# Performance work log

Measured on AMD Instinct MI355X. Metric: run time of the kernel, lower is better.

## Reference

```python
import jax, jax.numpy as jnp
import numpy as np

B, S, D, H, I, E, K, L, C = 4, 1024, 512, 8, 2048, 8, 2, 4, 4
D2 = D // 2
EPS = 1e-5  # torch LayerNorm default


def _ln(x, w, b):
    m = jnp.mean(x, -1, keepdims=True)
    v = jnp.mean((x - m) ** 2, -1, keepdims=True)
    return (x - m) * jax.lax.rsqrt(v + EPS) * w + b


def setup_inputs() -> dict:
    key = jax.random.key(0)
    ks = iter(jax.random.split(key, 40))
    n = lambda shp, s=0.02: jax.random.normal(next(ks), shp, dtype=jnp.float32) * s
    return {
        'embeddings': jax.random.normal(next(ks), (B, S, D), jnp.float32),
        'attention_mask': jnp.ones((B, S), jnp.float32),
        'in_w': n((L, 3 * D, D)), 'in_b': jnp.zeros((L, 3 * D)),
        'out_w': n((L, D, D)), 'out_b': jnp.zeros((L, D)),
        'ln1_w': jnp.ones((L, D)), 'ln1_b': jnp.zeros((L, D)),
        'ln2_w': jnp.ones((L, D)), 'ln2_b': jnp.zeros((L, D)),
        'gate_w': n((L, E, D)),
        'e_w1': n((L, E, D, I)), 'e_b1': jnp.zeros((L, E, I)),
        'e_w2': n((L, E, I, D)), 'e_b2': jnp.zeros((L, E, D)),
        'mln_w': jnp.ones((L, D)), 'mln_b': jnp.zeros((L, D)),
        'fln_w': jnp.ones((D,)), 'fln_b': jnp.zeros((D,)),
        'pool_w': n((D, D)), 'pool_b': jnp.zeros((D,)),
        'cls_w': n((C, D)), 'cls_b': jnp.zeros((C,)),
        'cf_w1': n((D2, D)), 'cf_b1': jnp.zeros((D2,)),
        'cf_w2': n((1, D2)), 'cf_b2': jnp.zeros((1,)),
    }


def _forward(embeddings, attention_mask, in_w, in_b, out_w, out_b, ln1_w, ln1_b,
             ln2_w, ln2_b, gate_w, e_w1, e_b1, e_w2, e_b2, mln_w, mln_b,
             fln_w, fln_b, pool_w, pool_b, cls_w, cls_b, cf_w1, cf_b1, cf_w2, cf_b2):
    x = embeddings
    dh = D // H
    total_aux = jnp.float32(0.0)
    for l in range(L):
        # --- self-attention (eval mode, dropout off) ---
        h = _ln(x, ln1_w[l], ln1_b[l])
        qkv = h @ in_w[l].T + in_b[l]                       # (B,S,3D)
        q, k, v = jnp.split(qkv, 3, axis=-1)
        q = q.reshape(B, S, H, dh).transpose(0, 2, 1, 3)
        k = k.reshape(B, S, H, dh).transpose(0, 2, 1, 3)
        v = v.reshape(B, S, H, dh).transpose(0, 2, 1, 3)
        scores = jnp.einsum('bhqd,bhkd->bhqk', q, k) / (dh ** 0.5)
        attn = jax.nn.softmax(scores, axis=-1)
        ctx = jnp.einsum('bhqk,bhkd->bhqd', attn, v).transpose(0, 2, 1, 3).reshape(B, S, D)
        x = x + (ctx @ out_w[l].T + out_b[l])
        # --- MoE FFN (residual is the post-norm2 tensor, per source) ---
        h = _ln(x, ln2_w[l], ln2_b[l])
        flat = h.reshape(-1, D)                             # (T,D)
        probs = jax.nn.softmax(flat @ gate_w[l].T, axis=-1) # (T,E)
        vals, idx = jax.lax.top_k(probs, K)                 # (T,K)
        vals = vals / vals.sum(-1, keepdims=True)
        onehot = jax.nn.one_hot(idx, E, dtype=flat.dtype)   # (T,K,E)
        comb = jnp.einsum('tk,tke->te', vals, onehot)       # (T,E) per-expert weight, 0 if not selected
        mid = jax.nn.gelu(jnp.einsum('td,edf->tef', flat, e_w1[l]) + e_b1[l], approximate=False)
        eout = jnp.einsum('tef,efd->ted', mid, e_w2[l]) + e_b2[l]
        moe_out = jnp.einsum('ted,te->td', eout, comb).reshape(B, S, D)
        moe_out = moe_out * attention_mask[..., None]
        x = _ln(h + moe_out, mln_w[l], mln_b[l])
        usage = onehot.sum((0, 1)) / flat.shape[0]
        total_aux = total_aux + jnp.mean((usage - 1.0 / E) ** 2)
    # --- head ---
    x = _ln(x, fln_w, fln_b)
    me = attention_mask[..., None]
    pooled = (x * me).sum(1) / jnp.maximum(me.sum(1), 1e-9)
    pooled = jnp.tanh(pooled @ pool_w.T + pool_b)
    logits = pooled @ cls_w.T + cls_b
    conf = jax.nn.sigmoid(jax.nn.relu(pooled @ cf_w1.T + cf_b1) @ cf_w2.T + cf_b2)
    return logits, total_aux / L, conf


def reference(embeddings, attention_mask, in_w, in_b, out_w, out_b, ln1_w, ln1_b,
              ln2_w, ln2_b, gate_w, e_w1, e_b1, e_w2, e_b2, mln_w, mln_b,
              fln_w, fln_b, pool_w, pool_b, cls_w, cls_b, cf_w1, cf_b1, cf_w2, cf_b2):
    return _forward(embeddings, attention_mask, in_w, in_b, out_w, out_b, ln1_w, ln1_b,
                    ln2_w, ln2_b, gate_w, e_w1, e_b1, e_w2, e_b2, mln_w, mln_b,
                    fln_w, fln_b, pool_w, pool_b, cls_w, cls_b, cf_w1, cf_b1, cf_w2, cf_b2)
```

## Files before the change

kernel.cpp:

```cpp
#include <hip/hip_runtime.h>
#include <math.h>

#define B_ 4
#define S_ 1024
#define D_ 512
#define H_ 8
#define DH_ 64
#define I_ 2048
#define E_ 8
#define L_ 4
#define T_ 4096

using bf16x8 = __attribute__((ext_vector_type(8))) __bf16;
using f32x4  = __attribute__((ext_vector_type(4))) float;

typedef __attribute__((address_space(1))) const void gvoid;
typedef __attribute__((address_space(3))) void lvoid;
__device__ __forceinline__ void gl_lds16(const void* g, void* l){
  __builtin_amdgcn_global_load_lds((gvoid*)g, (lvoid*)l, 16, 0, 0);
}

__device__ __forceinline__ float wred_sum(float v){
#pragma unroll
  for(int m=32;m>0;m>>=1) v += __shfl_xor(v, m, 64);
  return v;
}
__device__ __forceinline__ unsigned short f2bf(float f){
  unsigned x = __float_as_uint(f);
  unsigned r = (x + 0x7FFFu + ((x>>16)&1u)) >> 16;
  return (unsigned short)r;
}
__device__ __forceinline__ float bf2f(unsigned short u){
  return __uint_as_float(((unsigned)u)<<16);
}
__device__ __forceinline__ unsigned pk2(float a, float b){
  return (unsigned)f2bf(a) | ((unsigned)f2bf(b)<<16);
}

template<int BM, int BN, bool MOE, bool GATHER, bool OUT_BF16, int ACT, bool ADD_IN>
__global__ __launch_bounds__(256)
void gemm_k(const unsigned short* __restrict__ A, const unsigned short* __restrict__ Bv,
            void* Cp, const float* __restrict__ bias, const float* addin,
            int M, int N, int K, int lda, int ldb, int ldc,
            int hdiv, long sAb, long sAh, long sBb, long sBh, long sCb, long sCh,
            float scale,
            const int* __restrict__ moff, const int* __restrict__ mcnt,
            const int* __restrict__ rowtok, const int* __restrict__ btab,
            long sBe, int biasStride)
{
  constexpr int BK = 64;
  constexpr int WM = BM/2, WN = BN/2, FM = WM/16, FNN = WN/16;
  constexpr int RPC = 2048/BK;
  constexpr int NA = BM/RPC, NB = BN/RPC;
  __shared__ unsigned short As[BM*BK];
  __shared__ unsigned short Bs[BN*BK];

  const int tid = threadIdx.x, wid = tid>>6, lane = tid&63;
  const int wy = wid>>1, wx = wid&1, ln16 = lane&15, q8 = (lane>>4)*8;
  int m0 = blockIdx.x*BM;
  const int n0 = blockIdx.y*BN;

  float* Cf = nullptr; unsigned short* Ch = nullptr;
  const float* biasp = bias;
  const unsigned short* Bp = Bv;
  int seg = 0, cnt = M;

  if constexpr (MOE){
    int tv = btab[blockIdx.x];
    if (tv < 0) return;
    int e = tv>>8;
    m0 = (tv&255)*BM;
    seg = moff[e]; cnt = mcnt[e];
    Bp = Bv + (long)e*sBe;
    if constexpr (OUT_BF16) Ch = (unsigned short*)Cp; else Cf = (float*)Cp;
    if (biasp) biasp += (long)e*biasStride;
  } else {
    int z = blockIdx.z, zb = z/hdiv, zh = z%hdiv;
    A  += (long)zb*sAb + (long)zh*sAh;
    Bp += (long)zb*sBb + (long)zh*sBh;
    long coff = (long)zb*sCb + (long)zh*sCh;
    if constexpr (OUT_BF16) Ch = (unsigned short*)Cp + coff; else Cf = ((float*)Cp) + coff;
    if constexpr (ADD_IN) addin += coff;
  }

  const int srow = tid >> 3;
  const int scol = (tid & 7) * 8;
  long ga[NA], gb[NB];
#pragma unroll
  for (int j=0; j<NA; j++){
    int r = m0 + j*RPC + srow;
    if constexpr (MOE){
      r = min(r, cnt-1);
      long gr = GATHER ? (long)rowtok[seg+r] : (long)(seg+r);
      ga[j] = gr*lda + scol;
    } else {
      ga[j] = (long)min(r, M-1)*lda + scol;
    }
  }
#pragma unroll
  for (int j=0; j<NB; j++){
    int bn = min(n0 + j*RPC + srow, N-1);
    gb[j] = (long)bn*ldb + scol;
  }

  f32x4 acc[FM][FNN];
#pragma unroll
  for(int i=0;i<FM;i++)
#pragma unroll
    for(int j=0;j<FNN;j++){ f32x4 z = {0.f,0.f,0.f,0.f}; acc[i][j] = z; }

  for (int k0 = 0; k0 < K; k0 += BK){
    __syncthreads();
#pragma unroll
    for (int j=0; j<NA; j++) gl_lds16(A + ga[j] + k0, As + j*2048 + wid*512);
#pragma unroll
    for (int j=0; j<NB; j++) gl_lds16(Bp + gb[j] + k0, Bs + j*2048 + wid*512);
    __syncthreads();
#pragma unroll
    for (int kk=0; kk<2; kk++){
      bf16x8 fa[FM], fb[FNN];
#pragma unroll
      for(int i=0;i<FM;i++) fa[i] = *(const bf16x8*)&As[(wy*WM + i*16 + ln16)*BK + kk*32 + q8];
#pragma unroll
      for(int j=0;j<FNN;j++) fb[j] = *(const bf16x8*)&Bs[(wx*WN + j*16 + ln16)*BK + kk*32 + q8];
#pragma unroll
      for(int i=0;i<FM;i++)
#pragma unroll
        for(int j=0;j<FNN;j++)
          acc[i][j] = __builtin_amdgcn_mfma_f32_16x16x32_bf16(fa[i], fb[j], acc[i][j], 0, 0, 0);
    }
  }

#pragma unroll
  for(int i=0;i<FM;i++){
    int mbase = m0 + wy*WM + i*16 + (lane>>4)*4;
#pragma unroll
    for(int j=0;j<FNN;j++){
      int n = n0 + wx*WN + j*16 + ln16;
      float bv = biasp ? biasp[n] : 0.f;
      f32x4 v = acc[i][j];
#pragma unroll
      for(int r=0;r<4;r++){
        int m = mbase + r;
        if (m < cnt){
          float x = v[r]*scale + bv;
          if constexpr (ACT == 1) x = 0.5f*x*(1.f + erff(x*0.70710678118654752f));
          long ci = (long)(MOE ? seg + m : m)*ldc + n;
          if constexpr (ADD_IN) x += addin[ci];
          if constexpr (OUT_BF16) Ch[ci] = f2bf(x);
          else Cf[ci] = x;
        }
      }
    }
  }
}

__global__ __launch_bounds__(256)
void flash_k(const unsigned short* __restrict__ qkvb, const unsigned short* __restrict__ Vt,
             unsigned short* __restrict__ ctx)
{
  __shared__ unsigned short Pl[4][16*72];
  const int qt = blockIdx.x, z = blockIdx.y, b = z>>3, h = z&7;
  const int wid = threadIdx.x>>6, lane = threadIdx.x&63;
  const int ln16 = lane&15, g = lane>>4;
  const int q0 = qt*64 + wid*16;
  unsigned short* Pw = &Pl[wid][0];

  const unsigned short* Qp = qkvb + (long)(b*1024 + q0 + ln16)*1536 + h*64 + g*8;
  bf16x8 qf0 = *(const bf16x8*)Qp;
  bf16x8 qf1 = *(const bf16x8*)(Qp + 32);
  const unsigned short* Kbase = qkvb + (long)b*1024*1536 + 512 + h*64 + g*8;
  const unsigned short* Vbase = Vt + (long)z*65536 + g*8;

  float m_s[4], l_s[4];
  f32x4 oacc[4];
#pragma unroll
  for(int r=0;r<4;r++){ m_s[r] = -1e30f; l_s[r] = 0.f; }
#pragma unroll
  for(int j=0;j<4;j++){ f32x4 zz = {0.f,0.f,0.f,0.f}; oacc[j] = zz; }

  for (int t = 0; t < 16; ++t){
    bf16x8 kf[4][2], vf[4][2];
#pragma unroll
    for(int j=0;j<4;j++){
      const unsigned short* kp = Kbase + (long)(t*64 + j*16 + ln16)*1536;
      kf[j][0] = *(const bf16x8*)kp;
      kf[j][1] = *(const bf16x8*)(kp + 32);
      const unsigned short* vp = Vbase + (long)(j*16 + ln16)*1024 + t*64;
      vf[j][0] = *(const bf16x8*)vp;
      vf[j][1] = *(const bf16x8*)(vp + 32);
    }
    f32x4 sacc[4];
#pragma unroll
    for(int j=0;j<4;j++){ f32x4 zz = {0.f,0.f,0.f,0.f}; sacc[j] = zz; }
#pragma unroll
    for(int j=0;j<4;j++){
      sacc[j] = __builtin_amdgcn_mfma_f32_16x16x32_bf16(qf0, kf[j][0], sacc[j], 0,0,0);
      sacc[j] = __builtin_amdgcn_mfma_f32_16x16x32_bf16(qf1, kf[j][1], sacc[j], 0,0,0);
    }
#pragma unroll
    for(int j=0;j<4;j++)
#pragma unroll
      for(int r=0;r<4;r++) sacc[j][r] *= 0.125f;
    float alpha[4];
#pragma unroll
    for(int r=0;r<4;r++){
      float mx = fmaxf(fmaxf(sacc[0][r], sacc[1][r]), fmaxf(sacc[2][r], sacc[3][r]));
#pragma unroll
      for(int m=1;m<16;m<<=1) mx = fmaxf(mx, __shfl_xor(mx, m, 64));
      float mn = fmaxf(m_s[r], mx);
      alpha[r] = __expf(m_s[r] - mn);
      m_s[r] = mn;
    }
#pragma unroll
    for(int j=0;j<4;j++)
#pragma unroll
      for(int r=0;r<4;r++) sacc[j][r] = __expf(sacc[j][r] - m_s[r]);
#pragma unroll
    for(int r=0;r<4;r++){
      float rs = sacc[0][r]+sacc[1][r]+sacc[2][r]+sacc[3][r];
#pragma unroll
      for(int m=1;m<16;m<<=1) rs += __shfl_xor(rs, m, 64);
      l_s[r] = l_s[r]*alpha[r] + rs;
    }
#pragma unroll
    for(int j=0;j<4;j++)
#pragma unroll
      for(int r=0;r<4;r++) oacc[j][r] *= alpha[r];
#pragma unroll
    for(int j=0;j<4;j++)
#pragma unroll
      for(int r=0;r<4;r++)
        Pw[(g*4+r)*72 + j*16 + ln16] = f2bf(sacc[j][r]);
    bf16x8 pf0 = *(const bf16x8*)&Pw[ln16*72 + g*8];
    bf16x8 pf1 = *(const bf16x8*)&Pw[ln16*72 + 32 + g*8];
#pragma unroll
    for(int j=0;j<4;j++){
      oacc[j] = __builtin_amdgcn_mfma_f32_16x16x32_bf16(pf0, vf[j][0], oacc[j], 0,0,0);
      oacc[j] = __builtin_amdgcn_mfma_f32_16x16x32_bf16(pf1, vf[j][1], oacc[j], 0,0,0);
    }
  }
#pragma unroll
  for(int r=0;r<4;r++){
    float inv = 1.f/l_s[r];
    long row = (long)(b*1024 + q0 + g*4 + r)*512 + h*64;
#pragma unroll
    for(int j=0;j<4;j++)
      ctx[row + j*16 + ln16] = f2bf(oacc[j][r]*inv);
  }
}

template<bool OUT_BF16>
__global__ __launch_bounds__(256)
void ln_w_k(const float* __restrict__ in, const float* __restrict__ w,
            const float* __restrict__ bb, void* __restrict__ outp)
{
  int row = blockIdx.x*4 + (threadIdx.x>>6), lane = threadIdx.x&63;
  const float4* p = (const float4*)(in + (long)row*512 + lane*8);
  float4 a = p[0], c = p[1];
  float s = a.x+a.y+a.z+a.w + c.x+c.y+c.z+c.w;
  float q = a.x*a.x+a.y*a.y+a.z*a.z+a.w*a.w + c.x*c.x+c.y*c.y+c.z*c.z+c.w*c.w;
  s = wred_sum(s); q = wred_sum(q);
  float mean = s*(1.f/512.f);
  float var  = q*(1.f/512.f) - mean*mean;
  float inv  = rsqrtf(var + 1e-5f);
  const float4* wp = (const float4*)(w + lane*8);
  const float4* bp = (const float4*)(bb + lane*8);
  float4 w0 = wp[0], w1 = wp[1], b0 = bp[0], b1 = bp[1];
  float o0 = (a.x-mean)*inv*w0.x + b0.x, o1 = (a.y-mean)*inv*w0.y + b0.y;
  float o2 = (a.z-mean)*inv*w0.z + b0.z, o3 = (a.w-mean)*inv*w0.w + b0.w;
  float o4 = (c.x-mean)*inv*w1.x + b1.x, o5 = (c.y-mean)*inv*w1.y + b1.y;
  float o6 = (c.z-mean)*inv*w1.z + b1.z, o7 = (c.w-mean)*inv*w1.w + b1.w;
  if constexpr (OUT_BF16){
    *(uint4*)((unsigned short*)outp + (long)row*512 + lane*8) =
      make_uint4(pk2(o0,o1), pk2(o2,o3), pk2(o4,o5), pk2(o6,o7));
  } else {
    float4* op = (float4*)((float*)outp + (long)row*512 + lane*8);
    op[0] = make_float4(o0,o1,o2,o3);
    op[1] = make_float4(o4,o5,o6,o7);
  }
}

__global__ __launch_bounds__(256)
void ln2route_k(const float* __restrict__ in, const float* __restrict__ w,
                const float* __restrict__ bb, unsigned short* __restrict__ h2,
                const float* __restrict__ gw,
                int* __restrict__ tok_e, float* __restrict__ tok_w)
{
  int tok = blockIdx.x*4 + (threadIdx.x>>6), lane = threadIdx.x&63;
  const float4* p = (const float4*)(in + (long)tok*512 + lane*8);
  float4 a = p[0], c = p[1];
  float s = a.x+a.y+a.z+a.w + c.x+c.y+c.z+c.w;
  float q = a.x*a.x+a.y*a.y+a.z*a.z+a.w*a.w + c.x*c.x+c.y*c.y+c.z*c.z+c.w*c.w;
  s = wred_sum(s); q = wred_sum(q);
  float mean = s*(1.f/512.f);
  float var  = q*(1.f/512.f) - mean*mean;
  float inv  = rsqrtf(var + 1e-5f);
  const float4* wp = (const float4*)(w + lane*8);
  const float4* bp = (const float4*)(bb + lane*8);
  float4 w0 = wp[0], w1 = wp[1], b0 = bp[0], b1 = bp[1];
  float o[8];
  o[0] = (a.x-mean)*inv*w0.x + b0.x; o[1] = (a.y-mean)*inv*w0.y + b0.y;
  o[2] = (a.z-mean)*inv*w0.z + b0.z; o[3] = (a.w-mean)*inv*w0.w + b0.w;
  o[4] = (c.x-mean)*inv*w1.x + b1.x; o[5] = (c.y-mean)*inv*w1.y + b1.y;
  o[6] = (c.z-mean)*inv*w1.z + b1.z; o[7] = (c.w-mean)*inv*w1.w + b1.w;
  *(uint4*)(h2 + (long)tok*512 + lane*8) =
    make_uint4(pk2(o[0],o[1]), pk2(o[2],o[3]), pk2(o[4],o[5]), pk2(o[6],o[7]));
  float lg[8];
#pragma unroll
  for(int e=0;e<8;e++){
    const float4* gr = (const float4*)(gw + e*512 + lane*8);
    float4 g0 = gr[0], g1 = gr[1];
    float d = o[0]*g0.x + o[1]*g0.y + o[2]*g0.z + o[3]*g0.w
            + o[4]*g1.x + o[5]*g1.y + o[6]*g1.z + o[7]*g1.w;
    lg[e] = wred_sum(d);
  }
  if (lane == 0){
    float mx = lg[0];
#pragma unroll
    for(int e=1;e<8;e++) mx = fmaxf(mx, lg[e]);
    float pr[8];
#pragma unroll
    for(int e=0;e<8;e++) pr[e] = expf(lg[e]-mx);
    int e0 = 0; float p0 = pr[0];
#pragma unroll
    for(int e=1;e<8;e++) if (pr[e] > p0){ p0 = pr[e]; e0 = e; }
    int e1 = -1; float p1 = -1.f;
#pragma unroll
    for(int e=0;e<8;e++) if (e != e0 && pr[e] > p1){ p1 = pr[e]; e1 = e; }
    float invp = 1.f/(p0+p1);
    tok_e[2*tok] = e0; tok_e[2*tok+1] = e1;
    tok_w[2*tok] = p0*invp; tok_w[2*tok+1] = p1*invp;
  }
}

__global__ __launch_bounds__(1024)
void plan_scatter_k(const int* __restrict__ tok_e, const float* __restrict__ tok_w,
                    int* __restrict__ offs, int* __restrict__ cnts, float* __restrict__ aux,
                    int* __restrict__ btab, int* __restrict__ btab64,
                    int* __restrict__ rowtok, float* __restrict__ roww, int* __restrict__ rowof)
{
  __shared__ int hist[8];
  __shared__ int offsS[8];
  __shared__ int base[8];
  const int t = threadIdx.x;
  if (t < 8) hist[t] = 0;
  __syncthreads();
  int e[8]; float w[8];
#pragma unroll
  for (int i=0;i<8;i++){
    e[i] = tok_e[t + i*1024];
    w[i] = tok_w[t + i*1024];
    atomicAdd(&hist[e[i]], 1);
  }
  __syncthreads();
  if (t == 0){
    int o = 0, idx = 0, idx2 = 0; float a = 0.f;
    for (int ee=0; ee<8; ee++){
      offsS[ee] = o;
      int c = hist[ee];
      o += c;
      float u = (float)c*(1.f/4096.f) - 0.125f;
      a += u*u;
      int nb = (c + 127) >> 7;
      for (int j=0;j<nb;j++) btab[idx++] = (ee<<8)|j;
      int nb2 = (c + 63) >> 6;
      for (int j=0;j<nb2;j++) btab64[idx2++] = (ee<<8)|j;
    }
    while (idx < 80) btab[idx++] = -1;
    while (idx2 < 144) btab64[idx2++] = -1;
    *aux += a*(1.f/8.f);
  }
  __syncthreads();
  if (t < 8){
    cnts[t] = hist[t];
    offs[t] = offsS[t];
    base[t] = offsS[t];
  }
  __syncthreads();
#pragma unroll
  for (int i=0;i<8;i++){
    int pos = atomicAdd(&base[e[i]], 1);
    int gi = t + i*1024;
    rowtok[pos] = gi>>1;
    roww[pos] = w[i];
    rowof[gi] = pos;
  }
}

__global__ __launch_bounds__(256)
void ln_moe_k(const float* __restrict__ eout, const int* __restrict__ rowof,
              const float* __restrict__ roww, const float* __restrict__ mask,
              const unsigned short* __restrict__ h2,
              const float* __restrict__ w, const float* __restrict__ bb,
              float* __restrict__ outp)
{
  int tok = blockIdx.x*4 + (threadIdx.x>>6), lane = threadIdx.x&63;
  int r0 = rowof[2*tok], r1 = rowof[2*tok+1];
  float w0w = roww[r0], w1w = roww[r1], mk = mask[tok];
  const float4* ap = (const float4*)(eout + (long)r0*512 + lane*8);
  const float4* bp2 = (const float4*)(eout + (long)r1*512 + lane*8);
  float4 a0 = ap[0], a1 = ap[1], c0 = bp2[0], c1 = bp2[1];
  uint4 hu = *(const uint4*)(h2 + (long)tok*512 + lane*8);
  const unsigned short* hh = (const unsigned short*)&hu;
  float v[8];
  v[0] = bf2f(hh[0]) + (a0.x*w0w + c0.x*w1w)*mk;
  v[1] = bf2f(hh[1]) + (a0.y*w0w + c0.y*w1w)*mk;
  v[2] = bf2f(hh[2]) + (a0.z*w0w + c0.z*w1w)*mk;
  v[3] = bf2f(hh[3]) + (a0.w*w0w + c0.w*w1w)*mk;
  v[4] = bf2f(hh[4]) + (a1.x*w0w + c1.x*w1w)*mk;
  v[5] = bf2f(hh[5]) + (a1.y*w0w + c1.y*w1w)*mk;
  v[6] = bf2f(hh[6]) + (a1.z*w0w + c1.z*w1w)*mk;
  v[7] = bf2f(hh[7]) + (a1.w*w0w + c1.w*w1w)*mk;
  float s = 0.f, q = 0.f;
#pragma unroll
  for(int i=0;i<8;i++){ s += v[i]; q += v[i]*v[i]; }
  s = wred_sum(s); q = wred_sum(q);
  float mean = s*(1.f/512.f);
  float var  = q*(1.f/512.f) - mean*mean;
  float inv  = rsqrtf(var + 1e-5f);
  const float4* wp = (const float4*)(w + lane*8);
  const float4* bpp = (const float4*)(bb + lane*8);
  float4 w0 = wp[0], w1 = wp[1], b0 = bpp[0], b1 = bpp[1];
  float wv[8] = {w0.x,w0.y,w0.z,w0.w,w1.x,w1.y,w1.z,w1.w};
  float bv[8] = {b0.x,b0.y,b0.z,b0.w,b1.x,b1.y,b1.z,b1.w};
  float4* op = (float4*)(outp + (long)tok*512 + lane*8);
  op[0] = make_float4((v[0]-mean)*inv*wv[0]+bv[0], (v[1]-mean)*inv*wv[1]+bv[1],
                      (v[2]-mean)*inv*wv[2]+bv[2], (v[3]-mean)*inv*wv[3]+bv[3]);
  op[1] = make_float4((v[4]-mean)*inv*wv[4]+bv[4], (v[5]-mean)*inv*wv[5]+bv[5],
                      (v[6]-mean)*inv*wv[6]+bv[6], (v[7]-mean)*inv*wv[7]+bv[7]);
}

__global__ __launch_bounds__(256)
void vt_k(const unsigned short* __restrict__ qkvb, unsigned short* __restrict__ Vt)
{
  __shared__ unsigned short tile[64][80];
  int z = blockIdx.y, b = z>>3, h = z&7;
  int t = threadIdx.x;
  int kk = t>>2, dd = (t&3)*16;
  int dd2 = t>>2, kk2 = (t&3)*16;
  for (int c = 0; c < 4; ++c){
    int k0 = (blockIdx.x*4 + c)*64;
    const unsigned short* p = qkvb + ((long)(b*1024 + k0 + kk))*1536 + 1024 + h*64 + dd;
    uint4 u0 = *(const uint4*)p, u1 = *(const uint4*)(p+8);
    __syncthreads();
    *(uint4*)&tile[kk][dd] = u0;
    *(uint4*)&tile[kk][dd+8] = u1;
    __syncthreads();
    uint4 o0, o1;
    unsigned short* s0 = (unsigned short*)&o0;
    unsigned short* s1 = (unsigned short*)&o1;
#pragma unroll
    for(int j=0;j<8;j++){ s0[j] = tile[kk2+j][dd2]; s1[j] = tile[kk2+8+j][dd2]; }
    unsigned short* o = Vt + (long)z*65536 + (long)dd2*1024 + k0 + kk2;
    *(uint4*)o = o0; *(uint4*)(o+8) = o1;
  }
}

__global__ __launch_bounds__(256)
void transpose_cast_k(const float* __restrict__ in, unsigned short* __restrict__ outp,
                      int R, int C, int ZL)
{
  __shared__ float tile[64][65];
  int t = threadIdx.x;
  int rr = t>>2, cc = (t&3)*16;
  int cc2 = t>>2, rr2 = (t&3)*16;
  int c0 = blockIdx.x*64, r0 = blockIdx.y*64;
  for (int zi = 0; zi < ZL; ++zi){
    long zoff = (long)(blockIdx.z*ZL + zi) * R * C;
    const float* pin = in + zoff + (long)(r0+rr)*C + c0 + cc;
    float4 v0=*(const float4*)pin, v1=*(const float4*)(pin+4), v2=*(const float4*)(pin+8), v3=*(const float4*)(pin+12);
    __syncthreads();
    tile[rr][cc+0]=v0.x; tile[rr][cc+1]=v0.y; tile[rr][cc+2]=v0.z; tile[rr][cc+3]=v0.w;
    tile[rr][cc+4]=v1.x; tile[rr][cc+5]=v1.y; tile[rr][cc+6]=v1.z; tile[rr][cc+7]=v1.w;
    tile[rr][cc+8]=v2.x; tile[rr][cc+9]=v2.y; tile[rr][cc+10]=v2.z; tile[rr][cc+11]=v2.w;
    tile[rr][cc+12]=v3.x; tile[rr][cc+13]=v3.y; tile[rr][cc+14]=v3.z; tile[rr][cc+15]=v3.w;
    __syncthreads();
    unsigned tmp[8];
#pragma unroll
    for(int jj=0;jj<8;jj++)
      tmp[jj] = pk2(tile[rr2+2*jj][cc2], tile[rr2+2*jj+1][cc2]);
    uint4* dst = (uint4*)(outp + zoff + (long)(c0+cc2)*R + r0 + rr2);
    dst[0] = make_uint4(tmp[0],tmp[1],tmp[2],tmp[3]);
    dst[1] = make_uint4(tmp[4],tmp[5],tmp[6],tmp[7]);
  }
}

__global__ __launch_bounds__(256)
void cast_bf16_k(const float* __restrict__ in, unsigned short* __restrict__ outp, int n8)
{
  for (int i = blockIdx.x*256 + threadIdx.x; i < n8; i += gridDim.x*256){
    const float4* p = (const float4*)(in + (long)i*8);
    float4 a = p[0], b = p[1];
    *(uint4*)(outp + (long)i*8) = make_uint4(pk2(a.x,a.y), pk2(a.z,a.w), pk2(b.x,b.y), pk2(b.z,b.w));
  }
}

__global__ __launch_bounds__(256)
void pool2_k(const float* __restrict__ h, const float* __restrict__ mask, float* __restrict__ pooled)
{
  int b = blockIdx.x, sc = blockIdx.y, t = threadIdx.x;
  float a0 = 0.f, a1 = 0.f;
  const float* mb = mask + b*1024 + sc*128;
  const float* hbase = h + ((long)b*1024 + sc*128)*512;
  for (int s = 0; s < 128; ++s){
    float mk = mb[s];
    const float* r = hbase + (long)s*512;
    a0 += r[t]*mk; a1 += r[t+256]*mk;
  }
  pooled[((b*8 + sc)*512) + t] = a0;
  pooled[((b*8 + sc)*512) + t + 256] = a1;
}

__global__ __launch_bounds__(256)
void head_final_k(const float* __restrict__ pooled, const float* __restrict__ mask,
                  const float* __restrict__ pool_w, const float* __restrict__ pool_b,
                  const float* __restrict__ cls_w, const float* __restrict__ cls_b,
                  const float* __restrict__ cf_w1, const float* __restrict__ cf_b1,
                  const float* __restrict__ cf_w2, const float* __restrict__ cf_b2,
                  const float* __restrict__ aux, float* __restrict__ out)
{
  int b = blockIdx.x, t = threadIdx.x, wid = t>>6, lane = t&63;
  __shared__ __align__(16) float pld[512];
  __shared__ __align__(16) float p2[512];
  __shared__ float red[4];
  float ds = 0.f;
  for(int s=t; s<1024; s+=256) ds += mask[b*1024 + s];
  ds = wred_sum(ds);
  if (lane==0) red[wid] = ds;
  __syncthreads();
  float denom = fmaxf(red[0]+red[1]+red[2]+red[3], 1e-9f);
  float s0 = 0.f, s1 = 0.f;
#pragma unroll
  for(int sc=0;sc<8;sc++){
    s0 += pooled[((b*8+sc)*512) + t];
    s1 += pooled[((b*8+sc)*512) + t + 256];
  }
  pld[t]     = s0/denom;
  pld[t+256] = s1/denom;
  __syncthreads();
#pragma unroll
  for(int jj=0;jj<2;jj++){
    int j = t + jj*256;
    const float4* wr = (const float4*)(pool_w + (long)j*512);
    float acc = 0.f;
    for(int i=0;i<128;i++){
      float4 w4 = wr[i]; float4 x4 = ((const float4*)pld)[i];
      acc += w4.x*x4.x + w4.y*x4.y + w4.z*x4.z + w4.w*x4.w;
    }
    p2[j] = tanhf(acc + pool_b[j]);
  }
  __syncthreads();
  if (t < 4){
    const float4* wr = (const float4*)(cls_w + (long)t*512);
    float acc = 0.f;
    for(int i=0;i<128;i++){
      float4 w4 = wr[i]; float4 x4 = ((const float4*)p2)[i];
      acc += w4.x*x4.x + w4.y*x4.y + w4.z*x4.z + w4.w*x4.w;
    }
    out[b*4 + t] = acc + cls_b[t];
  }
  {
    const float4* wr = (const float4*)(cf_w1 + (long)t*512);
    float acc = 0.f;
    for(int i=0;i<128;i++){
      float4 w4 = wr[i]; float4 x4 = ((const float4*)p2)[i];
      acc += w4.x*x4.x + w4.y*x4.y + w4.z*x4.z + w4.w*x4.w;
    }
    acc = fmaxf(acc + cf_b1[t], 0.f) * cf_w2[t];
    acc = wred_sum(acc);
    __syncthreads();
    if (lane==0) red[wid] = acc;
    __syncthreads();
    if (t == 0){
      float sum = red[0]+red[1]+red[2]+red[3];
      out[17 + b] = 1.f/(1.f + expf(-(sum + cf_b2[0])));
    }
  }
  if (b == 0 && t == 0) out[16] = aux[0]*0.25f;
}

extern "C" void kernel_launch(void* const* d_in, const int* in_sizes, int n_in,
                              void* d_out, int out_size, void* d_ws, size_t ws_size,
                              hipStream_t stream)
{
  (void)in_sizes; (void)n_in; (void)out_size;
  const float* emb    = (const float*)d_in[0];
  const float* mask   = (const float*)d_in[1];
  const float* in_w   = (const float*)d_in[2];
  const float* in_b   = (const float*)d_in[3];
  const float* out_w  = (const float*)d_in[4];
  const float* out_b  = (const float*)d_in[5];
  const float* ln1_w  = (const float*)d_in[6];
  const float* ln1_b  = (const float*)d_in[7];
  const float* ln2_w  = (const float*)d_in[8];
  const float* ln2_b  = (const float*)d_in[9];
  const float* gate_w = (const float*)d_in[10];
  const float* e_w1   = (const float*)d_in[11];
  const float* e_b1   = (const float*)d_in[12];
  const float* e_w2   = (const float*)d_in[13];
  const float* e_b2   = (const float*)d_in[14];
  const float* mln_w  = (const float*)d_in[15];
  const float* mln_b  = (const float*)d_in[16];
  const float* fln_w  = (const float*)d_in[17];
  const float* fln_b  = (const float*)d_in[18];
  const float* pool_w = (const float*)d_in[19];
  const float* pool_b = (const float*)d_in[20];
  const float* cls_w  = (const float*)d_in[21];
  const float* cls_b  = (const float*)d_in[22];
  const float* cf_w1  = (const float*)d_in[23];
  const float* cf_b1  = (const float*)d_in[24];
  const float* cf_w2  = (const float*)d_in[25];
  const float* cf_b2  = (const float*)d_in[26];
  float* out = (float*)d_out;
  char* ws = (char*)d_ws;

  const size_t MiB = 1024*1024;
  if (ws_size < 218*MiB) return;

  float*          x     = (float*)(ws + 0*MiB);
  unsigned short* hb    = (unsigned short*)(ws + 8*MiB);
  unsigned short* qkvb  = (unsigned short*)(ws + 12*MiB);
  unsigned short* ctx   = (unsigned short*)(ws + 24*MiB);
  unsigned short* Vt    = (unsigned short*)(ws + 28*MiB);
  unsigned short* mid   = (unsigned short*)(ws + 32*MiB);
  float*          eout  = (float*)(ws + 64*MiB);
  float*          fout  = (float*)(ws + 64*MiB);
  unsigned short* w1t   = (unsigned short*)(ws + 80*MiB);
  unsigned short* w2t   = (unsigned short*)(ws + 144*MiB);
  unsigned short* inwb  = (unsigned short*)(ws + 208*MiB);
  unsigned short* outwb = (unsigned short*)(ws + 214*MiB);
  char* misc = ws + 216*MiB;
  int*   counts  = (int*)(misc + 0);
  int*   offs    = (int*)(misc + 64);
  float* aux     = (float*)(misc + 128);
  int*   btab    = (int*)(misc + 256);
  int*   btab64  = (int*)(misc + 1024);
  float* pooled  = (float*)(misc + 4096);
  int*   tok_e   = (int*)(misc + 81920);
  float* tok_w   = (float*)(misc + 114688);
  int*   rowtok  = (int*)(misc + 147456);
  float* roww    = (float*)(misc + 180224);
  int*   rowof   = (int*)(misc + 212992);

  hipMemcpyAsync(x, emb, (size_t)T_*D_*4, hipMemcpyDeviceToDevice, stream);
  hipMemsetAsync(aux, 0, 4, stream);
  cast_bf16_k<<<512, 256, 0, stream>>>(in_w, inwb, L_*3*D_*D_/8);
  cast_bf16_k<<<256, 256, 0, stream>>>(out_w, outwb, L_*D_*D_/8);
  transpose_cast_k<<<dim3(I_/64, D_/64, 4), 256, 0, stream>>>(e_w1, w1t, D_, I_, 8);
  transpose_cast_k<<<dim3(D_/64, I_/64, 4), 256, 0, stream>>>(e_w2, w2t, I_, D_, 8);

  for (int l=0; l<L_; l++){
    const float* inbl  = in_b  + (size_t)l*3*D_;
    const float* outbl = out_b + (size_t)l*D_;
    const float* gwl   = gate_w + (size_t)l*E_*D_;
    const float* eb1l  = e_b1 + (size_t)l*E_*I_;
    const float* eb2l  = e_b2 + (size_t)l*E_*D_;
    const unsigned short* inwbl  = inwb + (size_t)l*3*D_*D_;
    const unsigned short* outwbl = outwb + (size_t)l*D_*D_;
    const unsigned short* w1tl = w1t + (size_t)l*E_*I_*D_;
    const unsigned short* w2tl = w2t + (size_t)l*E_*D_*I_;

    ln_w_k<true><<<T_/4, 256, 0, stream>>>(x, ln1_w + (size_t)l*D_, ln1_b + (size_t)l*D_, hb);
    gemm_k<64,128,false,false,true,0,false><<<dim3(64,12,1), 256, 0, stream>>>(
      hb, inwbl, qkvb, inbl, nullptr, T_, 3*D_, D_, D_, D_, 3*D_,
      1, 0,0,0,0,0,0, 1.f, nullptr, nullptr, nullptr, nullptr, 0, 0);
    vt_k<<<dim3(4,32), 256, 0, stream>>>(qkvb, Vt);
    flash_k<<<dim3(16,32), 256, 0, stream>>>(qkvb, Vt, ctx);
    gemm_k<64,64,false,false,false,0,true><<<dim3(64,8,1), 256, 0, stream>>>(
      ctx, outwbl, x, outbl, x, T_, D_, D_, D_, D_, D_,
      1, 0,0,0,0,0,0, 1.f, nullptr, nullptr, nullptr, nullptr, 0, 0);
    ln2route_k<<<T_/4, 256, 0, stream>>>(x, ln2_w + (size_t)l*D_, ln2_b + (size_t)l*D_,
                                         hb, gwl, tok_e, tok_w);
    plan_scatter_k<<<1, 1024, 0, stream>>>(tok_e, tok_w, offs, counts, aux, btab, btab64,
                                           rowtok, roww, rowof);
    gemm_k<128,128,true,true,true,1,false><<<dim3(71,16,1), 256, 0, stream>>>(
      hb, w1tl, mid, eb1l, nullptr, 2*T_, I_, D_, D_, D_, I_,
      1, 0,0,0,0,0,0, 1.f, offs, counts, rowtok, btab, (long)I_*D_, I_);
    gemm_k<64,128,true,false,false,0,false><<<dim3(136,4,1), 256, 0, stream>>>(
      mid, w2tl, eout, eb2l, nullptr, 2*T_, D_, I_, I_, I_, D_,
      1, 0,0,0,0,0,0, 1.f, offs, counts, nullptr, btab64, (long)D_*I_, D_);
    ln_moe_k<<<T_/4, 256, 0, stream>>>(eout, rowof, roww, mask, hb,
                                       mln_w + (size_t)l*D_, mln_b + (size_t)l*D_, x);
  }
  ln_w_k<false><<<T_/4, 256, 0, stream>>>(x, fln_w, fln_b, fout);
  pool2_k<<<dim3(4,8), 256, 0, stream>>>(fout, mask, pooled);
  head_final_k<<<4, 256, 0, stream>>>(pooled, mask, pool_w, pool_b, cls_w, cls_b,
                                      cf_w1, cf_b1, cf_w2, cf_b2, aux, out);
}
```

Measured before the change: 1.503 ms.

## Double-buffer GEMM LDS tiles and remap workgroups across XCDs

The GEMM kernel now double-buffers its A and B LDS tiles. The next K-tile's global-to-LDS loads are issued before computing on the current tile, with explicit vmcnt waits and barriers, so load latency overlaps MFMA work. Launches are flattened to a 1D grid and the block index is remapped so that consecutive tiles land on the same XCD (stride of 8) for better L2 locality. This doubles LDS use per block, which may lower occupancy, and the hand-placed waitcnt and barrier logic adds the risk of subtle synchronization errors.

```diff
diff --git a/kernel.cpp b/kernel.cpp
--- a/kernel.cpp
+++ b/kernel.cpp
@@ -46,19 +46,26 @@
             float scale,
             const int* __restrict__ moff, const int* __restrict__ mcnt,
             const int* __restrict__ rowtok, const int* __restrict__ btab,
-            long sBe, int biasStride)
+            long sBe, int biasStride, int nby)
 {
   constexpr int BK = 64;
   constexpr int WM = BM/2, WN = BN/2, FM = WM/16, FNN = WN/16;
   constexpr int RPC = 2048/BK;
   constexpr int NA = BM/RPC, NB = BN/RPC;
-  __shared__ unsigned short As[BM*BK];
-  __shared__ unsigned short Bs[BN*BK];
+  constexpr int NLD = NA + NB;
+  __shared__ unsigned short As[2*BM*BK];
+  __shared__ unsigned short Bs[2*BN*BK];
 
   const int tid = threadIdx.x, wid = tid>>6, lane = tid&63;
   const int wy = wid>>1, wx = wid&1, ln16 = lane&15, q8 = (lane>>4)*8;
-  int m0 = blockIdx.x*BM;
-  const int n0 = blockIdx.y*BN;
+
+  const int nwg = gridDim.x, cpx = nwg >> 3;
+  const int lin = blockIdx.x;
+  const int wg  = (lin & 7)*cpx + (lin >> 3);
+  const int bxi = wg / nby, byi = wg % nby;
+
+  int m0 = bxi*BM;
+  const int n0 = byi*BN;
 
   float* Cf = nullptr; unsigned short* Ch = nullptr;
   const float* biasp = bias;
@@ -66,7 +73,7 @@
   int seg = 0, cnt = M;
 
   if constexpr (MOE){
-    int tv = btab[blockIdx.x];
+    int tv = btab[bxi];
     if (tv < 0) return;
     int e = tv>>8;
     m0 = (tv&255)*BM;
@@ -109,26 +116,44 @@
 #pragma unroll
     for(int j=0;j<FNN;j++){ f32x4 z = {0.f,0.f,0.f,0.f}; acc[i][j] = z; }
 
-  for (int k0 = 0; k0 < K; k0 += BK){
-    __syncthreads();
-#pragma unroll
-    for (int j=0; j<NA; j++) gl_lds16(A + ga[j] + k0, As + j*2048 + wid*512);
-#pragma unroll
-    for (int j=0; j<NB; j++) gl_lds16(Bp + gb[j] + k0, Bs + j*2048 + wid*512);
-    __syncthreads();
+  const int nt = K/BK;
+  int cur = 0;
+#pragma unroll
+  for (int j=0; j<NA; j++) gl_lds16(A + ga[j], As + j*2048 + wid*512);
+#pragma unroll
+  for (int j=0; j<NB; j++) gl_lds16(Bp + gb[j], Bs + j*2048 + wid*512);
+
+  for (int t = 0; t < nt; ++t){
+    const int cb = cur;
+    if (t+1 < nt){
+      const int nb2 = cur^1;
+      const int k0 = (t+1)*BK;
+#pragma unroll
+      for (int j=0; j<NA; j++) gl_lds16(A + ga[j] + k0, As + nb2*BM*BK + j*2048 + wid*512);
+#pragma unroll
+      for (int j=0; j<NB; j++) gl_lds16(Bp + gb[j] + k0, Bs + nb2*BN*BK + j*2048 + wid*512);
+      asm volatile("s_waitcnt vmcnt(%0)" :: "n"(NLD) : "memory");
+    } else {
+      asm volatile("s_waitcnt vmcnt(0)" ::: "memory");
+    }
+    __builtin_amdgcn_s_barrier();
+    __builtin_amdgcn_sched_barrier(0);
 #pragma unroll
     for (int kk=0; kk<2; kk++){
       bf16x8 fa[FM], fb[FNN];
 #pragma unroll
-      for(int i=0;i<FM;i++) fa[i] = *(const bf16x8*)&As[(wy*WM + i*16 + ln16)*BK + kk*32 + q8];
-#pragma unroll
-      for(int j=0;j<FNN;j++) fb[j] = *(const bf16x8*)&Bs[(wx*WN + j*16 + ln16)*BK + kk*32 + q8];
+      for(int i=0;i<FM;i++) fa[i] = *(const bf16x8*)&As[cb*BM*BK + (wy*WM + i*16 + ln16)*BK + kk*32 + q8];
+#pragma unroll
+      for(int j=0;j<FNN;j++) fb[j] = *(const bf16x8*)&Bs[cb*BN*BK + (wx*WN + j*16 + ln16)*BK + kk*32 + q8];
 #pragma unroll
       for(int i=0;i<FM;i++)
 #pragma unroll
         for(int j=0;j<FNN;j++)
           acc[i][j] = __builtin_amdgcn_mfma_f32_16x16x32_bf16(fa[i], fb[j], acc[i][j], 0, 0, 0);
     }
+    __builtin_amdgcn_sched_barrier(0);
+    __builtin_amdgcn_s_barrier();
+    cur ^= 1;
   }
 
 #pragma unroll
@@ -662,24 +687,24 @@
     const unsigned short* w2tl = w2t + (size_t)l*E_*D_*I_;
 
     ln_w_k<true><<<T_/4, 256, 0, stream>>>(x, ln1_w + (size_t)l*D_, ln1_b + (size_t)l*D_, hb);
-    gemm_k<64,128,false,false,true,0,false><<<dim3(64,12,1), 256, 0, stream>>>(
+    gemm_k<64,128,false,false,true,0,false><<<dim3(768,1,1), 256, 0, stream>>>(
       hb, inwbl, qkvb, inbl, nullptr, T_, 3*D_, D_, D_, D_, 3*D_,
-      1, 0,0,0,0,0,0, 1.f, nullptr, nullptr, nullptr, nullptr, 0, 0);
+      1, 0,0,0,0,0,0, 1.f, nullptr, nullptr, nullptr, nullptr, 0, 0, 12);
     vt_k<<<dim3(4,32), 256, 0, stream>>>(qkvb, Vt);
     flash_k<<<dim3(16,32), 256, 0, stream>>>(qkvb, Vt, ctx);
-    gemm_k<64,64,false,false,false,0,true><<<dim3(64,8,1), 256, 0, stream>>>(
+    gemm_k<64,64,false,false,false,0,true><<<dim3(512,1,1), 256, 0, stream>>>(
       ctx, outwbl, x, outbl, x, T_, D_, D_, D_, D_, D_,
-      1, 0,0,0,0,0,0, 1.f, nullptr, nullptr, nullptr, nullptr, 0, 0);
+      1, 0,0,0,0,0,0, 1.f, nullptr, nullptr, nullptr, nullptr, 0, 0, 8);
     ln2route_k<<<T_/4, 256, 0, stream>>>(x, ln2_w + (size_t)l*D_, ln2_b + (size_t)l*D_,
                                          hb, gwl, tok_e, tok_w);
     plan_scatter_k<<<1, 1024, 0, stream>>>(tok_e, tok_w, offs, counts, aux, btab, btab64,
                                            rowtok, roww, rowof);
-    gemm_k<128,128,true,true,true,1,false><<<dim3(71,16,1), 256, 0, stream>>>(
+    gemm_k<128,128,true,true,true,1,false><<<dim3(1136,1,1), 256, 0, stream>>>(
       hb, w1tl, mid, eb1l, nullptr, 2*T_, I_, D_, D_, D_, I_,
-      1, 0,0,0,0,0,0, 1.f, offs, counts, rowtok, btab, (long)I_*D_, I_);
-    gemm_k<64,128,true,false,false,0,false><<<dim3(136,4,1), 256, 0, stream>>>(
+      1, 0,0,0,0,0,0, 1.f, offs, counts, rowtok, btab, (long)I_*D_, I_, 16);
+    gemm_k<64,128,true,false,false,0,false><<<dim3(544,1,1), 256, 0, stream>>>(
       mid, w2tl, eout, eb2l, nullptr, 2*T_, D_, I_, I_, I_, D_,
-      1, 0,0,0,0,0,0, 1.f, offs, counts, nullptr, btab64, (long)D_*I_, D_);
+      1, 0,0,0,0,0,0, 1.f, offs, counts, nullptr, btab64, (long)D_*I_, D_, 4);
     ln_moe_k<<<T_/4, 256, 0, stream>>>(eout, rowof, roww, mask, hb,
                                        mln_w + (size_t)l*D_, mln_b + (size_t)l*D_, x);
   }
```

Result: no change. 1.490 ms (-0.8%).
